# Performance work log

Measured on AMD Instinct MI355X. Metric: run time of the kernel, lower is better.

Reference implementation:

```python
import jax, jax.numpy as jnp
import numpy as np

MEL, EMB, PRE, RNN, ATT = 80, 256, 256, 1024, 128
LOC_FILTERS, LOC_KERNEL = 32, 31


def _dropout(x, p, key):
    keep = jax.random.bernoulli(key, 1.0 - p, x.shape)
    return jnp.where(keep, x / (1.0 - p), 0.0).astype(x.dtype)


def _lstm_cell(x, h, c, Wih, Whh, bih, bhh):
    # torch LSTMCell gate order: i, f, g, o
    gates = x @ Wih.T + h @ Whh.T + (bih + bhh)
    i, f, g, o = jnp.split(gates, 4, axis=-1)
    c_new = jax.nn.sigmoid(f) * c + jax.nn.sigmoid(i) * jnp.tanh(g)
    h_new = jax.nn.sigmoid(o) * jnp.tanh(c_new)
    return h_new, c_new


def setup_inputs() -> dict:
    key = jax.random.key(0)
    ks = jax.random.split(key, 24)
    r = lambda k, shape, fan: (jax.random.normal(k, shape, jnp.float32) / np.sqrt(fan))
    inp = {
        "embedding": jax.random.normal(ks[0], (32, 512, EMB), jnp.float32),
        "target_mels": jax.random.uniform(ks[1], (32, 400, MEL), jnp.float32),
        # PreNet
        "W1": r(ks[2], (PRE, MEL), MEL), "b1": jnp.zeros((PRE,), jnp.float32),
        "W2": r(ks[3], (PRE, PRE), PRE), "b2": jnp.zeros((PRE,), jnp.float32),
        # pre_rnn LSTMCell: input = pre_net_dim + embedding_dim = 512
        "Wih_pre": r(ks[4], (4 * RNN, PRE + EMB), PRE + EMB),
        "Whh_pre": r(ks[5], (4 * RNN, RNN), RNN),
        "bih_pre": jnp.zeros((4 * RNN,), jnp.float32),
        "bhh_pre": jnp.zeros((4 * RNN,), jnp.float32),
        # location-sensitive attention
        "Wq": r(ks[6], (ATT, RNN), RNN),
        "Wmem": r(ks[7], (ATT, EMB), EMB),
        "conv_w": r(ks[8], (LOC_FILTERS, 2, LOC_KERNEL), 2 * LOC_KERNEL),
        "Wloc": r(ks[9], (ATT, LOC_FILTERS), LOC_FILTERS),
        "v": r(ks[10], (ATT,), ATT),
        # post_rnn LSTMCell: input = rnn_dim + embedding_dim = 1280
        "Wih_post": r(ks[11], (4 * RNN, RNN + EMB), RNN + EMB),
        "Whh_post": r(ks[12], (4 * RNN, RNN), RNN),
        "bih_post": jnp.zeros((4 * RNN,), jnp.float32),
        "bhh_post": jnp.zeros((4 * RNN,), jnp.float32),
        # projections
        "Wmel": r(ks[13], (MEL, RNN + EMB), RNN + EMB), "bmel": jnp.zeros((MEL,), jnp.float32),
        "Wstop": r(ks[14], (1, RNN + EMB), RNN + EMB), "bstop": jnp.zeros((1,), jnp.float32),
    }
    return inp


def _decoder_forward(embedding, target_mels, W1, b1, W2, b2,
                     Wih_pre, Whh_pre, bih_pre, bhh_pre,
                     Wq, Wmem, conv_w, Wloc, v,
                     Wih_post, Whh_post, bih_post, bhh_post,
                     Wmel, bmel, Wstop, bstop):
    B, S, _ = embedding.shape
    T = target_mels.shape[1]
    # precompute processed memory [B, S, ATT]
    mem_proj = jnp.einsum("bse,ae->bsa", embedding, Wmem)
    # teacher-forced previous frames: zeros GO frame then target_mels[:, :-1]
    prev = jnp.concatenate([jnp.zeros((B, 1, MEL), target_mels.dtype), target_mels[:, :-1]], axis=1)
    prev = jnp.transpose(prev, (1, 0, 2))  # [T, B, MEL]
    base_key = jax.random.key(42)

    def step(carry, xs):
        c_pre, h_pre, c_post, h_post, context, a_w, a_sum = carry
        mel_prev, t = xs
        k1, k2, k3, k4 = jax.random.split(jax.random.fold_in(base_key, t), 4)
        # PreNet (dropout always on, p=0.5)
        p = _dropout(jax.nn.relu(mel_prev @ W1.T + b1), 0.5, k1)
        p = _dropout(jax.nn.relu(p @ W2.T + b2), 0.5, k2)
        # pre_rnn -- note original swaps (c, h) state names; replicated faithfully
        x = jnp.concatenate([p, context], axis=-1)
        c_pre, h_pre = _lstm_cell(x, c_pre, h_pre, Wih_pre, Whh_pre, bih_pre, bhh_pre)
        c_pre = _dropout(c_pre, 0.1, k3)
        # location-sensitive attention; query = h_pre (as in source)
        align_cat = jnp.stack([a_sum, a_w], axis=1)  # [B, 2, S]
        loc = jax.lax.conv_general_dilated(
            align_cat, conv_w, window_strides=(1,),
            padding=[(LOC_KERNEL // 2, LOC_KERNEL // 2)],
            dimension_numbers=("NCH", "OIH", "NCH"))  # [B, 32, S]
        q = h_pre @ Wq.T  # [B, ATT]
        loc_proj = jnp.einsum("bcs,ac->bsa", loc, Wloc)
        energies = jnp.einsum("bsa,a->bs", jnp.tanh(q[:, None, :] + mem_proj + loc_proj), v)
        a_w = jax.nn.softmax(energies, axis=-1)  # [B, S]
        context = jnp.einsum("bs,bse->be", a_w, embedding)
        a_sum = a_sum + a_w
        # post_rnn (same swapped-state convention)
        x2 = jnp.concatenate([h_pre, context], axis=-1)
        c_post, h_post = _lstm_cell(x2, c_post, h_post, Wih_post, Whh_post, bih_post, bhh_post)
        c_post = _dropout(c_post, 0.1, k4)
        out = jnp.concatenate([h_post, context], axis=-1)
        mel = jax.nn.sigmoid(out @ Wmel.T + bmel)
        stop = jax.nn.sigmoid(out @ Wstop.T + bstop)
        return (c_pre, h_pre, c_post, h_post, context, a_w, a_sum), (mel, stop)

    z = lambda d: jnp.zeros((B, d), embedding.dtype)
    carry0 = (z(RNN), z(RNN), z(RNN), z(RNN), z(EMB),
              jnp.zeros((B, S), embedding.dtype), jnp.zeros((B, S), embedding.dtype))
    _, (mels, stops) = jax.lax.scan(step, carry0, (prev, jnp.arange(T)))
    mel_frames = jnp.transpose(mels, (1, 0, 2))   # [B, T, MEL]
    stop_values = jnp.transpose(stops, (1, 0, 2))  # [B, T, 1]
    return mel_frames, stop_values


def reference(embedding, target_mels, W1, b1, W2, b2,
              Wih_pre, Whh_pre, bih_pre, bhh_pre,
              Wq, Wmem, conv_w, Wloc, v,
              Wih_post, Whh_post, bih_post, bhh_post,
              Wmel, bmel, Wstop, bstop):
    return _decoder_forward(embedding, target_mels, W1, b1, W2, b2,
                            Wih_pre, Whh_pre, bih_pre, bhh_pre,
                            Wq, Wmem, conv_w, Wloc, v,
                            Wih_post, Whh_post, bih_post, bhh_post,
                            Wmel, bmel, Wstop, bstop)
```

## Files before the change

### kernel.cpp

```cpp
#include <hip/hip_runtime.h>
#include <cstdint>
#include <cstddef>


#define JAX_THREEFRY_PARTITIONABLE 1

#define BB   32
#define SS   512
#define EMBD 256
#define MELD 80
#define PRED 256
#define RNND 1024
#define ATTD 128
#define TT   400

__device__ __forceinline__ void tf_block(uint32_t k0, uint32_t k1,
                                         uint32_t x0, uint32_t x1,
                                         uint32_t& o0, uint32_t& o1) {
  uint32_t ks2 = k0 ^ k1 ^ 0x1BD11BDAu;
  x0 += k0; x1 += k1;
#define TFR(r) { x0 += x1; x1 = (x1 << (r)) | (x1 >> (32 - (r))); x1 ^= x0; }
  TFR(13) TFR(15) TFR(26) TFR(6)
  x0 += k1;  x1 += ks2 + 1u;
  TFR(17) TFR(29) TFR(16) TFR(24)
  x0 += ks2; x1 += k0 + 2u;
  TFR(13) TFR(15) TFR(26) TFR(6)
  x0 += k0;  x1 += k1 + 3u;
  TFR(17) TFR(29) TFR(16) TFR(24)
  x0 += k1;  x1 += ks2 + 4u;
  TFR(13) TFR(15) TFR(26) TFR(6)
  x0 += ks2; x1 += k0 + 5u;
#undef TFR
  o0 = x0; o1 = x1;
}

__device__ __forceinline__ void subkey(int t, int j, uint32_t& k0, uint32_t& k1) {
  uint32_t a, b;
  tf_block(0u, 42u, 0u, (uint32_t)t, a, b);
#if JAX_THREEFRY_PARTITIONABLE
  tf_block(a, b, 0u, (uint32_t)j, k0, k1);
#else
  uint32_t base = (uint32_t)((j & 1) * 2);
  uint32_t w = (uint32_t)(j >> 1);
  uint32_t p0, p1, q0, q1;
  tf_block(a, b, base,     base + 4u, p0, p1);
  tf_block(a, b, base + 1u, base + 5u, q0, q1);
  k0 = w ? p1 : p0;
  k1 = w ? q1 : q0;
#endif
}

__device__ __forceinline__ bool keep_draw(uint32_t k0, uint32_t k1,
                                          uint32_t idx, uint32_t n, float pkeep) {
  uint32_t bits;
#if JAX_THREEFRY_PARTITIONABLE
  uint32_t o0, o1;
  tf_block(k0, k1, 0u, idx, o0, o1);
  bits = o0 ^ o1;
#else
  uint32_t half = n >> 1;
  uint32_t o0, o1;
  if (idx < half) { tf_block(k0, k1, idx, idx + half, o0, o1); bits = o0; }
  else            { tf_block(k0, k1, idx - half, idx, o0, o1); bits = o1; }
#endif
  float u = __uint_as_float((bits >> 9) | 0x3f800000u) - 1.0f;
  return u < pkeep;
}

__device__ __forceinline__ float sigm(float x) { return 1.0f / (1.0f + expf(-x)); }

__global__ void zero_kernel(float* p, int n) {
  int i = blockIdx.x * blockDim.x + threadIdx.x;
  if (i < n) p[i] = 0.0f;
}

__global__ __launch_bounds__(256) void prenet_kernel(
    const float* __restrict__ tmels, const float* __restrict__ W1,
    const float* __restrict__ b1, const float* __restrict__ W2,
    const float* __restrict__ b2, float* __restrict__ P_all) {
  __shared__ float melsh[MELD];
  __shared__ float h1sh[PRED];
  int blk = blockIdx.x, tid = threadIdx.x;
  int t = blk >> 5, b = blk & 31;
  if (tid < MELD)
    melsh[tid] = (t == 0) ? 0.0f : tmels[((size_t)b * TT + (t - 1)) * MELD + tid];
  __syncthreads();
  uint32_t k10, k11, k20, k21;
  subkey(t, 0, k10, k11);
  subkey(t, 1, k20, k21);
  {
    const float* wr = W1 + (size_t)tid * MELD;
    float acc = b1[tid];
    for (int m = 0; m < MELD; ++m) acc += melsh[m] * wr[m];
    acc = fmaxf(acc, 0.0f);
    bool kp = keep_draw(k10, k11, (uint32_t)(b * PRED + tid), BB * PRED, 0.5f);
    h1sh[tid] = kp ? (acc / 0.5f) : 0.0f;
  }
  __syncthreads();
  {
    const float* wr = W2 + (size_t)tid * PRED;
    float acc = b2[tid];
    for (int k = 0; k < PRED; ++k) acc += h1sh[k] * wr[k];
    acc = fmaxf(acc, 0.0f);
    bool kp = keep_draw(k20, k21, (uint32_t)(b * PRED + tid), BB * PRED, 0.5f);
    P_all[((size_t)t * BB + b) * PRED + tid] = kp ? (acc / 0.5f) : 0.0f;
  }
}

__global__ __launch_bounds__(128) void memproj_kernel(
    const float* __restrict__ emb, const float* __restrict__ Wmem,
    float* __restrict__ mp) {
  __shared__ float esh[EMBD];
  int blk = blockIdx.x, tid = threadIdx.x;
  const float* er = emb + (size_t)blk * EMBD;
  esh[tid] = er[tid];
  esh[tid + 128] = er[tid + 128];
  __syncthreads();
  const float4* wr = (const float4*)(Wmem + (size_t)tid * EMBD);
  const float4* xr = (const float4*)esh;
  float acc = 0.0f;
  for (int k4 = 0; k4 < EMBD / 4; ++k4) {
    float4 w = wr[k4], x = xr[k4];
    acc += w.x * x.x + w.y * x.y + w.z * x.z + w.w * x.w;
  }
  mp[(size_t)blk * ATTD + tid] = acc;
}

__global__ __launch_bounds__(256) void combo_kernel(
    int t, int do1, int do2,
    const float* __restrict__ P_all,
    const float* __restrict__ ctx_r,
    const float* __restrict__ Apre_r, const float* __restrict__ Bpre_r,
    float* __restrict__ Apre_w, float* __restrict__ Bpre_w,
    const float* __restrict__ Wih_pre, const float* __restrict__ Whh_pre,
    const float* __restrict__ bih_pre, const float* __restrict__ bhh_pre,
    const float* __restrict__ Apost_r, const float* __restrict__ Bpost_r,
    float* __restrict__ Apost_w, float* __restrict__ Bpost_w,
    const float* __restrict__ Wih_post, const float* __restrict__ Whh_post,
    const float* __restrict__ bih_post, const float* __restrict__ bhh_post) {
  __shared__ float xs[BB][256];
  const int blk = blockIdx.x;
  const int tid = threadIdx.x;
  const bool is1 = (blk < 128);
  if (is1 ? !do1 : !do2) return;
  const int tstep = is1 ? t : (t - 1);
  const int hb = (is1 ? blk : blk - 128) * 8;
  const int col = tid & 31;
  const int lq  = tid >> 5;
  const int b0  = lq * 4;
  const int gate = col >> 3;
  const int hl   = col & 7;
  const int gcol = gate * RNND + hb + hl;
  const int nchunks = is1 ? 6 : 9;

  float acc0 = 0.f, acc1 = 0.f, acc2 = 0.f, acc3 = 0.f;

  for (int ch = 0; ch < nchunks; ++ch) {
    __syncthreads();
#pragma unroll
    for (int it = 0; it < 8; ++it) {
      int flat = tid + it * 256;
      int bb = flat >> 6;
      int k4 = flat & 63;
      const float* src;
      if (is1) {
        if (ch == 0)      src = P_all + ((size_t)t * BB + bb) * PRED;
        else if (ch == 1) src = ctx_r + (size_t)bb * EMBD;
        else              src = Apre_r + (size_t)bb * RNND + (ch - 2) * 256;
      } else {
        if (ch < 4)       src = Bpre_r + (size_t)bb * RNND + ch * 256;
        else if (ch == 4) src = ctx_r + (size_t)bb * EMBD;
        else              src = Apost_r + (size_t)bb * RNND + (ch - 5) * 256;
      }
      float4 v4 = *(((const float4*)src) + k4);
      *(((float4*)&xs[bb][0]) + k4) = v4;
    }
    __syncthreads();

    const float* wrow;
    if (is1) wrow = (ch < 2) ? (Wih_pre + (size_t)gcol * 512 + ch * 256)
                             : (Whh_pre + (size_t)gcol * 1024 + (ch - 2) * 256);
    else     wrow = (ch < 5) ? (Wih_post + (size_t)gcol * 1280 + ch * 256)
                             : (Whh_post + (size_t)gcol * 1024 + (ch - 5) * 256);
    const float4* w4p = (const float4*)wrow;
#pragma unroll 8
    for (int k4 = 0; k4 < 64; ++k4) {
      float4 w = w4p[k4];
      float4 xa = *(((const float4*)&xs[b0 + 0][0]) + k4);
      float4 xb = *(((const float4*)&xs[b0 + 1][0]) + k4);
      float4 xc = *(((const float4*)&xs[b0 + 2][0]) + k4);
      float4 xd = *(((const float4*)&xs[b0 + 3][0]) + k4);
      acc0 += w.x * xa.x + w.y * xa.y + w.z * xa.z + w.w * xa.w;
      acc1 += w.x * xb.x + w.y * xb.y + w.z * xb.z + w.w * xb.w;
      acc2 += w.x * xc.x + w.y * xc.y + w.z * xc.z + w.w * xc.w;
      acc3 += w.x * xd.x + w.y * xd.y + w.z * xd.z + w.w * xd.w;
    }
  }

  float bsum = is1 ? (bih_pre[gcol] + bhh_pre[gcol])
                   : (bih_post[gcol] + bhh_post[gcol]);
  acc0 += bsum; acc1 += bsum; acc2 += bsum; acc3 += bsum;

  int lane = tid & 63;
  float f0 = __shfl(acc0, lane + 8),  f1 = __shfl(acc1, lane + 8);
  float f2 = __shfl(acc2, lane + 8),  f3 = __shfl(acc3, lane + 8);
  float g0 = __shfl(acc0, lane + 16), g1 = __shfl(acc1, lane + 16);
  float g2 = __shfl(acc2, lane + 16), g3 = __shfl(acc3, lane + 16);
  float q0 = __shfl(acc0, lane + 24), q1 = __shfl(acc1, lane + 24);
  float q2 = __shfl(acc2, lane + 24), q3 = __shfl(acc3, lane + 24);

  if (gate == 0) {
    uint32_t kk0, kk1;
    subkey(tstep, is1 ? 2 : 3, kk0, kk1);
    const int h = hb + hl;
    const float* Bold = is1 ? Bpre_r : Bpost_r;
    float* Aw = is1 ? Apre_w : Apost_w;
    float* Bw = is1 ? Bpre_w : Bpost_w;
    float ia[4] = {acc0, acc1, acc2, acc3};
    float fa[4] = {f0, f1, f2, f3};
    float ga[4] = {g0, g1, g2, g3};
    float oa[4] = {q0, q1, q2, q3};
#pragma unroll
    for (int i2 = 0; i2 < 4; ++i2) {
      int bb = b0 + i2;
      float iv = sigm(ia[i2]);
      float fv = sigm(fa[i2]);
      float gv = tanhf(ga[i2]);
      float ov = sigm(oa[i2]);
      float c_new = fv * Bold[(size_t)bb * RNND + h] + iv * gv;
      float h_new = ov * tanhf(c_new);
      bool kp = keep_draw(kk0, kk1, (uint32_t)(bb * RNND + h), BB * RNND, 0.9f);
      Aw[(size_t)bb * RNND + h] = kp ? (h_new / 0.9f) : 0.0f;
      Bw[(size_t)bb * RNND + h] = c_new;
    }
  }
}

__global__ __launch_bounds__(256) void q_kernel(
    const float* __restrict__ Bpre_new, const float* __restrict__ Wq,
    float* __restrict__ qout) {
  __shared__ float xsh[2][RNND];
  int blk = blockIdx.x, tid = threadIdx.x;
  int b2 = blk * 2;
  for (int flat = tid; flat < 2 * RNND; flat += 256)
    xsh[flat >> 10][flat & 1023] =
        Bpre_new[(size_t)(b2 + (flat >> 10)) * RNND + (flat & 1023)];
  __syncthreads();
  int a = tid & 127, bh = tid >> 7;
  const float4* wr = (const float4*)(Wq + (size_t)a * RNND);
  const float4* xr = (const float4*)&xsh[bh][0];
  float acc = 0.0f;
  for (int k4 = 0; k4 < RNND / 4; ++k4) {
    float4 w = wr[k4], x = xr[k4];
    acc += w.x * x.x + w.y * x.y + w.z * x.z + w.w * x.w;
  }
  qout[(size_t)(b2 + bh) * ATTD + a] = acc;
}

__global__ __launch_bounds__(256) void att_kernel(
    int do_att, int do_out, int t_prev,
    const float* __restrict__ qin, const float* __restrict__ memproj,
    const float* __restrict__ aw_r, const float* __restrict__ asum_r,
    const float* __restrict__ conv_w, const float* __restrict__ Wloc,
    const float* __restrict__ vvec, float* __restrict__ energ,
    const float* __restrict__ Bpost_o, const float* __restrict__ ctx_o,
    const float* __restrict__ Wmel, const float* __restrict__ bmel,
    const float* __restrict__ Wstop, const float* __restrict__ bstop,
    float* __restrict__ dout) {
  int blk = blockIdx.x, tid = threadIdx.x;
  if (blk >= 256) {
    if (!do_out) return;
    int b = blk - 256;
    int o = tid;
    if (o > 80) return;
    const float* wrow = (o < 80) ? (Wmel + (size_t)o * 1280) : Wstop;
    const float4* w4 = (const float4*)wrow;
    const float4* x4 = (const float4*)(Bpost_o + (size_t)b * RNND);
    float acc = 0.0f;
    for (int k4 = 0; k4 < RNND / 4; ++k4) {
      float4 w = w4[k4], x = x4[k4];
      acc += w.x * x.x + w.y * x.y + w.z * x.z + w.w * x.w;
    }
    const float4* w4b = (const float4*)(wrow + RNND);
    const float4* c4 = (const float4*)(ctx_o + (size_t)b * EMBD);
    for (int k4 = 0; k4 < EMBD / 4; ++k4) {
      float4 w = w4b[k4], x = c4[k4];
      acc += w.x * x.x + w.y * x.y + w.z * x.z + w.w * x.w;
    }
    acc += (o < 80) ? bmel[o] : bstop[0];
    float val = sigm(acc);
    if (o < 80) dout[(size_t)b * (TT * MELD) + (size_t)t_prev * MELD + o] = val;
    else        dout[(size_t)BB * TT * MELD + (size_t)b * TT + t_prev] = val;
    return;
  }
  if (!do_att) return;
  __shared__ float qsh[ATTD];
  __shared__ float vsh[ATTD];
  __shared__ float awin[94], aswin[94];
  __shared__ float wlocs[ATTD * 33];
  __shared__ float convs[32 * 62];
  __shared__ float locs[64 * 33];
  int b = blk >> 3, st = blk & 7, s0 = st * 64;
  if (tid < ATTD) { qsh[tid] = qin[b * ATTD + tid]; vsh[tid] = vvec[tid]; }
  if (tid < 94) {
    int sg = s0 - 15 + tid;
    bool ok = (sg >= 0) && (sg < SS);
    awin[tid]  = ok ? aw_r[b * SS + sg]   : 0.0f;
    aswin[tid] = ok ? asum_r[b * SS + sg] : 0.0f;
  }
  for (int idx = tid; idx < ATTD * 32; idx += 256) {
    int a = idx >> 5, c = idx & 31;
    wlocs[a * 33 + c] = Wloc[a * 32 + c];
  }
  for (int idx = tid; idx < 32 * 62; idx += 256) convs[idx] = conv_w[idx];
  __syncthreads();
  for (int idx = tid; idx < 64 * 32; idx += 256) {
    int sl = idx & 63, c = idx >> 6;
    const float* cw0 = &convs[c * 62];
    const float* cw1 = &convs[c * 62 + 31];
    float acc = 0.0f;
    for (int k = 0; k < 31; ++k)
      acc += cw0[k] * aswin[sl + k] + cw1[k] * awin[sl + k];
    locs[sl * 33 + c] = acc;
  }
  __syncthreads();
  int sl = tid >> 2, aq = tid & 3, sg = s0 + sl;
  const float* mp = memproj + ((size_t)b * SS + sg) * ATTD;
  float acc = 0.0f;
  const float* ls = &locs[sl * 33];
  for (int j = 0; j < 32; ++j) {
    int a = j * 4 + aq;
    const float* wl = &wlocs[a * 33];
    float lp = 0.0f;
#pragma unroll 8
    for (int c = 0; c < 32; ++c) lp += ls[c] * wl[c];
    acc += vsh[a] * tanhf(qsh[a] + mp[a] + lp);
  }
  acc += __shfl_down(acc, 2);
  acc += __shfl_down(acc, 1);
  if (aq == 0) energ[b * SS + sg] = acc;
}

__global__ __launch_bounds__(256) void sm_ctx_kernel(
    const float* __restrict__ energ, const float* __restrict__ emb,
    const float* __restrict__ asum_r, float* __restrict__ aw_w,
    float* __restrict__ asum_w, float* __restrict__ ctx_w) {
  __shared__ float psh[SS];
  __shared__ float red[256];
  __shared__ float cpart[4][64];
  int blk = blockIdx.x, tid = threadIdx.x;
  int b = blk >> 2, ec = blk & 3;
  float e1 = energ[b * SS + tid], e2 = energ[b * SS + 256 + tid];
  red[tid] = fmaxf(e1, e2);
  __syncthreads();
  for (int s = 128; s > 0; s >>= 1) {
    if (tid < s) red[tid] = fmaxf(red[tid], red[tid + s]);
    __syncthreads();
  }
  float mx = red[0];
  __syncthreads();
  float p1 = expf(e1 - mx), p2 = expf(e2 - mx);
  psh[tid] = p1; psh[tid + 256] = p2;
  red[tid] = p1 + p2;
  __syncthreads();
  for (int s = 128; s > 0; s >>= 1) {
    if (tid < s) red[tid] += red[tid + s];
    __syncthreads();
  }
  float inv = 1.0f / red[0];
  int el = tid & 63, sq = tid >> 6;
  int e = ec * 64 + el;
  float acc = 0.0f;
  const float* ebase = emb + ((size_t)b * SS) * EMBD + e;
  for (int s = sq * 128; s < sq * 128 + 128; ++s)
    acc += psh[s] * ebase[(size_t)s * EMBD];
  cpart[sq][el] = acc;
  __syncthreads();
  if (tid < 64)
    ctx_w[b * EMBD + ec * 64 + tid] =
        (cpart[0][tid] + cpart[1][tid] + cpart[2][tid] + cpart[3][tid]) * inv;
  if (ec == 0) {
    float a1 = p1 * inv, a2 = p2 * inv;
    aw_w[b * SS + tid] = a1;
    aw_w[b * SS + 256 + tid] = a2;
    asum_w[b * SS + tid] = asum_r[b * SS + tid] + a1;
    asum_w[b * SS + 256 + tid] = asum_r[b * SS + 256 + tid] + a2;
  }
}

extern "C" void kernel_launch(void* const* d_in, const int* in_sizes, int n_in,
                              void* d_out, int out_size, void* d_ws, size_t ws_size,
                              hipStream_t stream) {
  const float* emb      = (const float*)d_in[0];
  const float* tmels    = (const float*)d_in[1];
  const float* W1       = (const float*)d_in[2];
  const float* b1       = (const float*)d_in[3];
  const float* W2       = (const float*)d_in[4];
  const float* b2       = (const float*)d_in[5];
  const float* Wih_pre  = (const float*)d_in[6];
  const float* Whh_pre  = (const float*)d_in[7];
  const float* bih_pre  = (const float*)d_in[8];
  const float* bhh_pre  = (const float*)d_in[9];
  const float* Wq       = (const float*)d_in[10];
  const float* Wmem     = (const float*)d_in[11];
  const float* conv_w   = (const float*)d_in[12];
  const float* Wloc     = (const float*)d_in[13];
  const float* vvec     = (const float*)d_in[14];
  const float* Wih_post = (const float*)d_in[15];
  const float* Whh_post = (const float*)d_in[16];
  const float* bih_post = (const float*)d_in[17];
  const float* bhh_post = (const float*)d_in[18];
  const float* Wmel     = (const float*)d_in[19];
  const float* bmel     = (const float*)d_in[20];
  const float* Wstop    = (const float*)d_in[21];
  const float* bstop    = (const float*)d_in[22];
  float* out = (float*)d_out;

  float* w = (float*)d_ws;
  size_t off = 0;
  auto carve = [&](size_t n) {
    float* p = w + off;
    off += (n + 63) & ~((size_t)63);
    return p;
  };
  float* memproj = carve((size_t)BB * SS * ATTD);
  float* P_all   = carve((size_t)TT * BB * PRED);
  size_t state_begin = off;
  float* Apre[2]  = {carve(BB * RNND), carve(BB * RNND)};
  float* Bpre[2]  = {carve(BB * RNND), carve(BB * RNND)};
  float* Apost[2] = {carve(BB * RNND), carve(BB * RNND)};
  float* Bpost[2] = {carve(BB * RNND), carve(BB * RNND)};
  float* ctx[2]   = {carve(BB * EMBD), carve(BB * EMBD)};
  float* aw[2]    = {carve(BB * SS), carve(BB * SS)};
  float* asum[2]  = {carve(BB * SS), carve(BB * SS)};
  size_t state_end = off;
  float* q     = carve(BB * ATTD);
  float* energ = carve(BB * SS);

  int nz = (int)(state_end - state_begin);
  zero_kernel<<<(nz + 255) / 256, 256, 0, stream>>>(w + state_begin, nz);

  prenet_kernel<<<TT * BB, 256, 0, stream>>>(tmels, W1, b1, W2, b2, P_all);
  memproj_kernel<<<BB * SS, 128, 0, stream>>>(emb, Wmem, memproj);

  for (int t = 0; t <= TT; ++t) {
    int r = t & 1, wr2 = 1 - r;
    combo_kernel<<<256, 256, 0, stream>>>(
        t, (int)(t < TT), (int)(t > 0),
        P_all, ctx[r], Apre[r], Bpre[r], Apre[wr2], Bpre[wr2],
        Wih_pre, Whh_pre, bih_pre, bhh_pre,
        Apost[wr2], Bpost[wr2], Apost[r], Bpost[r],
        Wih_post, Whh_post, bih_post, bhh_post);
    if (t < TT) {
      q_kernel<<<16, 256, 0, stream>>>(Bpre[wr2], Wq, q);
      att_kernel<<<288, 256, 0, stream>>>(
          1, (int)(t > 0), t - 1,
          q, memproj, aw[r], asum[r], conv_w, Wloc, vvec, energ,
          Bpost[r], ctx[r], Wmel, bmel, Wstop, bstop, out);
      sm_ctx_kernel<<<128, 256, 0, stream>>>(
          energ, emb, asum[r], aw[wr2], asum[wr2], ctx[wr2]);
    } else {
      att_kernel<<<288, 256, 0, stream>>>(
          0, 1, t - 1,
          q, memproj, aw[r], asum[r], conv_w, Wloc, vvec, energ,
          Bpost[r], ctx[r], Wmel, bmel, Wstop, bstop, out);
    }
  }
  (void)in_sizes; (void)n_in; (void)out_size; (void)ws_size;
}
```

Before: 79.72 ms.

## Fuse per-step decoder kernels into one persistent kernel with grid barriers

Replaces the roughly 1600 per-timestep kernel launches (combo, q, attention, softmax/context) with a single persistent 256-block kernel. It loops over timesteps internally and separates phases with an atomic-counter grid barrier. The goal is to remove per-launch overhead and inter-kernel gaps on this latency-bound recurrent loop. It relies on all 256 blocks being co-resident, and the spin barriers add their own synchronisation cost. The non-partitionable threefry path is also removed.

```diff
diff --git a/kernel.cpp b/kernel.cpp
--- a/kernel.cpp
+++ b/kernel.cpp
@@ -2,8 +2,6 @@
 #include <cstdint>
 #include <cstddef>
 
-
-#define JAX_THREEFRY_PARTITIONABLE 1
 
 #define BB   32
 #define SS   512
@@ -13,6 +11,7 @@
 #define RNND 1024
 #define ATTD 128
 #define TT   400
+#define NBLK 256
 
 __device__ __forceinline__ void tf_block(uint32_t k0, uint32_t k1,
                                          uint32_t x0, uint32_t x1,
@@ -37,41 +36,44 @@
 __device__ __forceinline__ void subkey(int t, int j, uint32_t& k0, uint32_t& k1) {
   uint32_t a, b;
   tf_block(0u, 42u, 0u, (uint32_t)t, a, b);
-#if JAX_THREEFRY_PARTITIONABLE
   tf_block(a, b, 0u, (uint32_t)j, k0, k1);
-#else
-  uint32_t base = (uint32_t)((j & 1) * 2);
-  uint32_t w = (uint32_t)(j >> 1);
-  uint32_t p0, p1, q0, q1;
-  tf_block(a, b, base,     base + 4u, p0, p1);
-  tf_block(a, b, base + 1u, base + 5u, q0, q1);
-  k0 = w ? p1 : p0;
-  k1 = w ? q1 : q0;
-#endif
 }
 
 __device__ __forceinline__ bool keep_draw(uint32_t k0, uint32_t k1,
-                                          uint32_t idx, uint32_t n, float pkeep) {
-  uint32_t bits;
-#if JAX_THREEFRY_PARTITIONABLE
+                                          uint32_t idx, float pkeep) {
   uint32_t o0, o1;
   tf_block(k0, k1, 0u, idx, o0, o1);
-  bits = o0 ^ o1;
-#else
-  uint32_t half = n >> 1;
-  uint32_t o0, o1;
-  if (idx < half) { tf_block(k0, k1, idx, idx + half, o0, o1); bits = o0; }
-  else            { tf_block(k0, k1, idx - half, idx, o0, o1); bits = o1; }
-#endif
+  uint32_t bits = o0 ^ o1;
   float u = __uint_as_float((bits >> 9) | 0x3f800000u) - 1.0f;
   return u < pkeep;
 }
 
 __device__ __forceinline__ float sigm(float x) { return 1.0f / (1.0f + expf(-x)); }
 
-__global__ void zero_kernel(float* p, int n) {
+__device__ __forceinline__ void gsync(uint32_t* cnt, uint32_t* gen, uint32_t& lgen) {
+  __threadfence();
+  __syncthreads();
+  lgen += 1u;
+  if (threadIdx.x == 0) {
+    uint32_t a = __hip_atomic_fetch_add(cnt, 1u, __ATOMIC_ACQ_REL,
+                                        __HIP_MEMORY_SCOPE_AGENT);
+    if (a == (uint32_t)(NBLK - 1)) {
+      __hip_atomic_store(cnt, 0u, __ATOMIC_RELAXED, __HIP_MEMORY_SCOPE_AGENT);
+      __hip_atomic_store(gen, lgen, __ATOMIC_RELEASE, __HIP_MEMORY_SCOPE_AGENT);
+    } else {
+      while (__hip_atomic_load(gen, __ATOMIC_ACQUIRE,
+                               __HIP_MEMORY_SCOPE_AGENT) < lgen) {
+        __builtin_amdgcn_s_sleep(2);
+      }
+    }
+  }
+  __syncthreads();
+}
+
+__global__ void init_kernel(float* statebase, int nstate, uint32_t* barrier2) {
   int i = blockIdx.x * blockDim.x + threadIdx.x;
-  if (i < n) p[i] = 0.0f;
+  if (i < nstate) statebase[i] = 0.0f;
+  if (i == 0) { barrier2[0] = 0u; barrier2[1] = 0u; }
 }
 
 __global__ __launch_bounds__(256) void prenet_kernel(
@@ -93,7 +95,7 @@
     float acc = b1[tid];
     for (int m = 0; m < MELD; ++m) acc += melsh[m] * wr[m];
     acc = fmaxf(acc, 0.0f);
-    bool kp = keep_draw(k10, k11, (uint32_t)(b * PRED + tid), BB * PRED, 0.5f);
+    bool kp = keep_draw(k10, k11, (uint32_t)(b * PRED + tid), 0.5f);
     h1sh[tid] = kp ? (acc / 0.5f) : 0.0f;
   }
   __syncthreads();
@@ -102,7 +104,7 @@
     float acc = b2[tid];
     for (int k = 0; k < PRED; ++k) acc += h1sh[k] * wr[k];
     acc = fmaxf(acc, 0.0f);
-    bool kp = keep_draw(k20, k21, (uint32_t)(b * PRED + tid), BB * PRED, 0.5f);
+    bool kp = keep_draw(k20, k21, (uint32_t)(b * PRED + tid), 0.5f);
     P_all[((size_t)t * BB + b) * PRED + tid] = kp ? (acc / 0.5f) : 0.0f;
   }
 }
@@ -126,345 +128,348 @@
   mp[(size_t)blk * ATTD + tid] = acc;
 }
 
-__global__ __launch_bounds__(256) void combo_kernel(
-    int t, int do1, int do2,
-    const float* __restrict__ P_all,
-    const float* __restrict__ ctx_r,
-    const float* __restrict__ Apre_r, const float* __restrict__ Bpre_r,
-    float* __restrict__ Apre_w, float* __restrict__ Bpre_w,
-    const float* __restrict__ Wih_pre, const float* __restrict__ Whh_pre,
-    const float* __restrict__ bih_pre, const float* __restrict__ bhh_pre,
-    const float* __restrict__ Apost_r, const float* __restrict__ Bpost_r,
-    float* __restrict__ Apost_w, float* __restrict__ Bpost_w,
-    const float* __restrict__ Wih_post, const float* __restrict__ Whh_post,
-    const float* __restrict__ bih_post, const float* __restrict__ bhh_post) {
-  __shared__ float xs[BB][256];
+struct DecParams {
+  const float *emb, *tmels;
+  const float *Wih_pre, *Whh_pre, *bih_pre, *bhh_pre;
+  const float *Wq, *conv_w, *Wloc, *vvec;
+  const float *Wih_post, *Whh_post, *bih_post, *bhh_post;
+  const float *Wmel, *bmel, *Wstop, *bstop;
+  float *out;
+  float *memproj, *P_all;
+  float *Apre0, *Apre1, *Bpre0, *Bpre1;
+  float *Apost0, *Apost1, *Bpost0, *Bpost1;
+  float *ctx0, *ctx1, *aw0, *aw1, *asum0, *asum1;
+  float *qbuf, *energ;
+  uint32_t *barrier2;
+};
+
+__global__ __launch_bounds__(256) void decoder_persistent(DecParams p) {
+  __shared__ __align__(16) float smem[8768];
   const int blk = blockIdx.x;
   const int tid = threadIdx.x;
-  const bool is1 = (blk < 128);
-  if (is1 ? !do1 : !do2) return;
-  const int tstep = is1 ? t : (t - 1);
-  const int hb = (is1 ? blk : blk - 128) * 8;
-  const int col = tid & 31;
-  const int lq  = tid >> 5;
-  const int b0  = lq * 4;
-  const int gate = col >> 3;
-  const int hl   = col & 7;
-  const int gcol = gate * RNND + hb + hl;
-  const int nchunks = is1 ? 6 : 9;
-
-  float acc0 = 0.f, acc1 = 0.f, acc2 = 0.f, acc3 = 0.f;
-
-  for (int ch = 0; ch < nchunks; ++ch) {
-    __syncthreads();
+  uint32_t* bcnt = p.barrier2;
+  uint32_t* bgen = p.barrier2 + 1;
+  uint32_t lgen = 0u;
+
+  for (int t = 0; t <= TT; ++t) {
+    const int rr = t & 1;
+    const float* Apre_r  = rr ? p.Apre1  : p.Apre0;
+    const float* Bpre_r  = rr ? p.Bpre1  : p.Bpre0;
+    float*       Apre_w  = rr ? p.Apre0  : p.Apre1;
+    float*       Bpre_w  = rr ? p.Bpre0  : p.Bpre1;
+    const float* Apost_r = rr ? p.Apost0 : p.Apost1;
+    const float* Bpost_r = rr ? p.Bpost0 : p.Bpost1;
+    float*       Apost_w = rr ? p.Apost1 : p.Apost0;
+    float*       Bpost_w = rr ? p.Bpost1 : p.Bpost0;
+    const float* ctx_r   = rr ? p.ctx1   : p.ctx0;
+    float*       ctx_w   = rr ? p.ctx0   : p.ctx1;
+    const float* aw_r    = rr ? p.aw1    : p.aw0;
+    float*       aw_w    = rr ? p.aw0    : p.aw1;
+    const float* asum_r  = rr ? p.asum1  : p.asum0;
+    float*       asum_w  = rr ? p.asum0  : p.asum1;
+
+    {
+      const bool is1 = (blk < 128);
+      const bool active = is1 ? (t < TT) : (t > 0);
+      if (active) {
+        float (*xs)[256] = (float (*)[256])smem;
+        const int tstep = is1 ? t : (t - 1);
+        const int hb = (is1 ? blk : blk - 128) * 8;
+        const int col = tid & 31;
+        const int lq  = tid >> 5;
+        const int b0  = lq * 4;
+        const int gate = col >> 3;
+        const int hl   = col & 7;
+        const int gcol = gate * RNND + hb + hl;
+        const int nchunks = is1 ? 6 : 9;
+
+        float acc0 = 0.f, acc1 = 0.f, acc2 = 0.f, acc3 = 0.f;
+
+        for (int ch = 0; ch < nchunks; ++ch) {
+          __syncthreads();
 #pragma unroll
-    for (int it = 0; it < 8; ++it) {
-      int flat = tid + it * 256;
-      int bb = flat >> 6;
-      int k4 = flat & 63;
-      const float* src;
-      if (is1) {
-        if (ch == 0)      src = P_all + ((size_t)t * BB + bb) * PRED;
-        else if (ch == 1) src = ctx_r + (size_t)bb * EMBD;
-        else              src = Apre_r + (size_t)bb * RNND + (ch - 2) * 256;
-      } else {
-        if (ch < 4)       src = Bpre_r + (size_t)bb * RNND + ch * 256;
-        else if (ch == 4) src = ctx_r + (size_t)bb * EMBD;
-        else              src = Apost_r + (size_t)bb * RNND + (ch - 5) * 256;
-      }
-      float4 v4 = *(((const float4*)src) + k4);
-      *(((float4*)&xs[bb][0]) + k4) = v4;
+          for (int it = 0; it < 8; ++it) {
+            int flat = tid + it * 256;
+            int bb = flat >> 6;
+            int k4 = flat & 63;
+            const float* src;
+            if (is1) {
+              if (ch == 0)      src = p.P_all + ((size_t)t * BB + bb) * PRED;
+              else if (ch == 1) src = ctx_r + (size_t)bb * EMBD;
+              else              src = Apre_r + (size_t)bb * RNND + (ch - 2) * 256;
+            } else {
+              if (ch < 4)       src = Bpre_r + (size_t)bb * RNND + ch * 256;
+              else if (ch == 4) src = ctx_r + (size_t)bb * EMBD;
+              else              src = Apost_r + (size_t)bb * RNND + (ch - 5) * 256;
+            }
+            float4 v4 = *(((const float4*)src) + k4);
+            *(((float4*)&xs[bb][0]) + k4) = v4;
+          }
+          __syncthreads();
+
+          const float* wrow;
+          if (is1) wrow = (ch < 2) ? (p.Wih_pre + (size_t)gcol * 512 + ch * 256)
+                                   : (p.Whh_pre + (size_t)gcol * 1024 + (ch - 2) * 256);
+          else     wrow = (ch < 5) ? (p.Wih_post + (size_t)gcol * 1280 + ch * 256)
+                                   : (p.Whh_post + (size_t)gcol * 1024 + (ch - 5) * 256);
+          const float4* w4p = (const float4*)wrow;
+#pragma unroll 8
+          for (int k4 = 0; k4 < 64; ++k4) {
+            float4 w = w4p[k4];
+            float4 xa = *(((const float4*)&xs[b0 + 0][0]) + k4);
+            float4 xb = *(((const float4*)&xs[b0 + 1][0]) + k4);
+            float4 xc = *(((const float4*)&xs[b0 + 2][0]) + k4);
+            float4 xd = *(((const float4*)&xs[b0 + 3][0]) + k4);
+            acc0 += w.x * xa.x + w.y * xa.y + w.z * xa.z + w.w * xa.w;
+            acc1 += w.x * xb.x + w.y * xb.y + w.z * xb.z + w.w * xb.w;
+            acc2 += w.x * xc.x + w.y * xc.y + w.z * xc.z + w.w * xc.w;
+            acc3 += w.x * xd.x + w.y * xd.y + w.z * xd.z + w.w * xd.w;
+          }
+        }
+
+        float bsum = is1 ? (p.bih_pre[gcol] + p.bhh_pre[gcol])
+                         : (p.bih_post[gcol] + p.bhh_post[gcol]);
+        acc0 += bsum; acc1 += bsum; acc2 += bsum; acc3 += bsum;
+
+        int lane = tid & 63;
+        float f0 = __shfl(acc0, lane + 8),  f1 = __shfl(acc1, lane + 8);
+        float f2 = __shfl(acc2, lane + 8),  f3 = __shfl(acc3, lane + 8);
+        float g0 = __shfl(acc0, lane + 16), g1 = __shfl(acc1, lane + 16);
+        float g2 = __shfl(acc2, lane + 16), g3 = __shfl(acc3, lane + 16);
+        float q0 = __shfl(acc0, lane + 24), q1 = __shfl(acc1, lane + 24);
+        float q2 = __shfl(acc2, lane + 24), q3 = __shfl(acc3, lane + 24);
+
+        if (gate == 0) {
+          uint32_t kk0, kk1;
+          subkey(tstep, is1 ? 2 : 3, kk0, kk1);
+          const int h = hb + hl;
+          const float* Bold = is1 ? Bpre_r : Bpost_r;
+          float* Aw = is1 ? Apre_w : Apost_w;
+          float* Bw = is1 ? Bpre_w : Bpost_w;
+          float ia[4] = {acc0, acc1, acc2, acc3};
+          float fa[4] = {f0, f1, f2, f3};
+          float ga[4] = {g0, g1, g2, g3};
+          float oa[4] = {q0, q1, q2, q3};
+#pragma unroll
+          for (int i2 = 0; i2 < 4; ++i2) {
+            int bb = b0 + i2;
+            float iv = sigm(ia[i2]);
+            float fv = sigm(fa[i2]);
+            float gv = tanhf(ga[i2]);
+            float ov = sigm(oa[i2]);
+            float c_new = fv * Bold[(size_t)bb * RNND + h] + iv * gv;
+            float h_new = ov * tanhf(c_new);
+            bool kp = keep_draw(kk0, kk1, (uint32_t)(bb * RNND + h), 0.9f);
+            Aw[(size_t)bb * RNND + h] = kp ? (h_new / 0.9f) : 0.0f;
+            Bw[(size_t)bb * RNND + h] = c_new;
+          }
+        }
+      }
     }
-    __syncthreads();
-
-    const float* wrow;
-    if (is1) wrow = (ch < 2) ? (Wih_pre + (size_t)gcol * 512 + ch * 256)
-                             : (Whh_pre + (size_t)gcol * 1024 + (ch - 2) * 256);
-    else     wrow = (ch < 5) ? (Wih_post + (size_t)gcol * 1280 + ch * 256)
-                             : (Whh_post + (size_t)gcol * 1024 + (ch - 5) * 256);
-    const float4* w4p = (const float4*)wrow;
+    gsync(bcnt, bgen, lgen);
+
+    if (blk < 16) {
+      if (t < TT) {
+        float* xsh = smem;
+        int b2 = blk * 2;
+        for (int flat = tid; flat < 2 * RNND; flat += 256)
+          xsh[flat] = Bpre_w[(size_t)(b2 + (flat >> 10)) * RNND + (flat & 1023)];
+        __syncthreads();
+        int a = tid & 127, bh = tid >> 7;
+        const float4* wr = (const float4*)(p.Wq + (size_t)a * RNND);
+        const float4* xr = ((const float4*)xsh) + bh * (RNND / 4);
+        float acc = 0.0f;
+        for (int k4 = 0; k4 < RNND / 4; ++k4) {
+          float4 w = wr[k4], x = xr[k4];
+          acc += w.x * x.x + w.y * x.y + w.z * x.z + w.w * x.w;
+        }
+        p.qbuf[(size_t)(b2 + bh) * ATTD + a] = acc;
+      }
+    } else if (blk < 48) {
+      if (t > 0) {
+        int b = blk - 16;
+        int o = tid;
+        int t_prev = t - 1;
+        if (o <= 80) {
+          const float* wrow = (o < 80) ? (p.Wmel + (size_t)o * 1280) : p.Wstop;
+          const float4* w4 = (const float4*)wrow;
+          const float4* x4 = (const float4*)(Bpost_w + (size_t)b * RNND);
+          float acc = 0.0f;
+          for (int k4 = 0; k4 < RNND / 4; ++k4) {
+            float4 w = w4[k4], x = x4[k4];
+            acc += w.x * x.x + w.y * x.y + w.z * x.z + w.w * x.w;
+          }
+          const float4* w4b = (const float4*)(wrow + RNND);
+          const float4* c4 = (const float4*)(ctx_r + (size_t)b * EMBD);
+          for (int k4 = 0; k4 < EMBD / 4; ++k4) {
+            float4 w = w4b[k4], x = c4[k4];
+            acc += w.x * x.x + w.y * x.y + w.z * x.z + w.w * x.w;
+          }
+          acc += (o < 80) ? p.bmel[o] : p.bstop[0];
+          float val = sigm(acc);
+          if (o < 80)
+            p.out[(size_t)b * (TT * MELD) + (size_t)t_prev * MELD + o] = val;
+          else
+            p.out[(size_t)BB * TT * MELD + (size_t)b * TT + t_prev] = val;
+        }
+      }
+    }
+    gsync(bcnt, bgen, lgen);
+
+    if (t < TT) {
+      float* qsh   = smem;
+      float* vsh   = smem + 128;
+      float* awin  = smem + 256;
+      float* aswin = smem + 352;
+      float* wlocs = smem + 448;
+      float* convs = smem + 4672;
+      float* locs  = smem + 6656;
+      int b = blk >> 3, st = blk & 7, s0 = st * 64;
+      __syncthreads();
+      if (tid < ATTD) { qsh[tid] = p.qbuf[b * ATTD + tid]; vsh[tid] = p.vvec[tid]; }
+      if (tid < 94) {
+        int sg = s0 - 15 + tid;
+        bool ok = (sg >= 0) && (sg < SS);
+        awin[tid]  = ok ? aw_r[b * SS + sg]   : 0.0f;
+        aswin[tid] = ok ? asum_r[b * SS + sg] : 0.0f;
+      }
+      for (int idx = tid; idx < ATTD * 32; idx += 256) {
+        int a = idx >> 5, c = idx & 31;
+        wlocs[a * 33 + c] = p.Wloc[a * 32 + c];
+      }
+      for (int idx = tid; idx < 32 * 62; idx += 256) convs[idx] = p.conv_w[idx];
+      __syncthreads();
+      for (int idx = tid; idx < 64 * 32; idx += 256) {
+        int sl = idx & 63, c = idx >> 6;
+        const float* cw0 = &convs[c * 62];
+        const float* cw1 = &convs[c * 62 + 31];
+        float acc = 0.0f;
+        for (int k = 0; k < 31; ++k)
+          acc += cw0[k] * aswin[sl + k] + cw1[k] * awin[sl + k];
+        locs[sl * 33 + c] = acc;
+      }
+      __syncthreads();
+      int sl = tid >> 2, aq = tid & 3, sg = s0 + sl;
+      const float* mp = p.memproj + ((size_t)b * SS + sg) * ATTD;
+      float acc = 0.0f;
+      const float* ls = &locs[sl * 33];
+      for (int j = 0; j < 32; ++j) {
+        int a = j * 4 + aq;
+        const float* wl = &wlocs[a * 33];
+        float lp = 0.0f;
 #pragma unroll 8
-    for (int k4 = 0; k4 < 64; ++k4) {
-      float4 w = w4p[k4];
-      float4 xa = *(((const float4*)&xs[b0 + 0][0]) + k4);
-      float4 xb = *(((const float4*)&xs[b0 + 1][0]) + k4);
-      float4 xc = *(((const float4*)&xs[b0 + 2][0]) + k4);
-      float4 xd = *(((const float4*)&xs[b0 + 3][0]) + k4);
-      acc0 += w.x * xa.x + w.y * xa.y + w.z * xa.z + w.w * xa.w;
-      acc1 += w.x * xb.x + w.y * xb.y + w.z * xb.z + w.w * xb.w;
-      acc2 += w.x * xc.x + w.y * xc.y + w.z * xc.z + w.w * xc.w;
-      acc3 += w.x * xd.x + w.y * xd.y + w.z * xd.z + w.w * xd.w;
+        for (int c = 0; c < 32; ++c) lp += ls[c] * wl[c];
+        acc += vsh[a] * tanhf(qsh[a] + mp[a] + lp);
+      }
+      acc += __shfl_down(acc, 2);
+      acc += __shfl_down(acc, 1);
+      if (aq == 0) p.energ[b * SS + sg] = acc;
     }
-  }
-
-  float bsum = is1 ? (bih_pre[gcol] + bhh_pre[gcol])
-                   : (bih_post[gcol] + bhh_post[gcol]);
-  acc0 += bsum; acc1 += bsum; acc2 += bsum; acc3 += bsum;
-
-  int lane = tid & 63;
-  float f0 = __shfl(acc0, lane + 8),  f1 = __shfl(acc1, lane + 8);
-  float f2 = __shfl(acc2, lane + 8),  f3 = __shfl(acc3, lane + 8);
-  float g0 = __shfl(acc0, lane + 16), g1 = __shfl(acc1, lane + 16);
-  float g2 = __shfl(acc2, lane + 16), g3 = __shfl(acc3, lane + 16);
-  float q0 = __shfl(acc0, lane + 24), q1 = __shfl(acc1, lane + 24);
-  float q2 = __shfl(acc2, lane + 24), q3 = __shfl(acc3, lane + 24);
-
-  if (gate == 0) {
-    uint32_t kk0, kk1;
-    subkey(tstep, is1 ? 2 : 3, kk0, kk1);
-    const int h = hb + hl;
-    const float* Bold = is1 ? Bpre_r : Bpost_r;
-    float* Aw = is1 ? Apre_w : Apost_w;
-    float* Bw = is1 ? Bpre_w : Bpost_w;
-    float ia[4] = {acc0, acc1, acc2, acc3};
-    float fa[4] = {f0, f1, f2, f3};
-    float ga[4] = {g0, g1, g2, g3};
-    float oa[4] = {q0, q1, q2, q3};
-#pragma unroll
-    for (int i2 = 0; i2 < 4; ++i2) {
-      int bb = b0 + i2;
-      float iv = sigm(ia[i2]);
-      float fv = sigm(fa[i2]);
-      float gv = tanhf(ga[i2]);
-      float ov = sigm(oa[i2]);
-      float c_new = fv * Bold[(size_t)bb * RNND + h] + iv * gv;
-      float h_new = ov * tanhf(c_new);
-      bool kp = keep_draw(kk0, kk1, (uint32_t)(bb * RNND + h), BB * RNND, 0.9f);
-      Aw[(size_t)bb * RNND + h] = kp ? (h_new / 0.9f) : 0.0f;
-      Bw[(size_t)bb * RNND + h] = c_new;
+    gsync(bcnt, bgen, lgen);
+
+    if (t < TT && blk < 128) {
+      float* psh   = smem;
+      float* red   = smem + 512;
+      float (*cpart)[64] = (float (*)[64])(smem + 768);
+      int b = blk >> 2, ec = blk & 3;
+      float e1 = p.energ[b * SS + tid], e2 = p.energ[b * SS + 256 + tid];
+      red[tid] = fmaxf(e1, e2);
+      __syncthreads();
+      for (int s = 128; s > 0; s >>= 1) {
+        if (tid < s) red[tid] = fmaxf(red[tid], red[tid + s]);
+        __syncthreads();
+      }
+      float mx = red[0];
+      __syncthreads();
+      float p1 = expf(e1 - mx), p2 = expf(e2 - mx);
+      psh[tid] = p1; psh[tid + 256] = p2;
+      red[tid] = p1 + p2;
+      __syncthreads();
+      for (int s = 128; s > 0; s >>= 1) {
+        if (tid < s) red[tid] += red[tid + s];
+        __syncthreads();
+      }
+      float inv = 1.0f / red[0];
+      int el = tid & 63, sq = tid >> 6;
+      int e = ec * 64 + el;
+      float acc = 0.0f;
+      const float* ebase = p.emb + ((size_t)b * SS) * EMBD + e;
+      for (int s = sq * 128; s < sq * 128 + 128; ++s)
+        acc += psh[s] * ebase[(size_t)s * EMBD];
+      cpart[sq][el] = acc;
+      __syncthreads();
+      if (tid < 64)
+        ctx_w[b * EMBD + ec * 64 + tid] =
+            (cpart[0][tid] + cpart[1][tid] + cpart[2][tid] + cpart[3][tid]) * inv;
+      if (ec == 0) {
+        float a1 = p1 * inv, a2 = p2 * inv;
+        aw_w[b * SS + tid] = a1;
+        aw_w[b * SS + 256 + tid] = a2;
+        asum_w[b * SS + tid] = asum_r[b * SS + tid] + a1;
+        asum_w[b * SS + 256 + tid] = asum_r[b * SS + 256 + tid] + a2;
+      }
     }
-  }
-}
-
-__global__ __launch_bounds__(256) void q_kernel(
-    const float* __restrict__ Bpre_new, const float* __restrict__ Wq,
-    float* __restrict__ qout) {
-  __shared__ float xsh[2][RNND];
-  int blk = blockIdx.x, tid = threadIdx.x;
-  int b2 = blk * 2;
-  for (int flat = tid; flat < 2 * RNND; flat += 256)
-    xsh[flat >> 10][flat & 1023] =
-        Bpre_new[(size_t)(b2 + (flat >> 10)) * RNND + (flat & 1023)];
-  __syncthreads();
-  int a = tid & 127, bh = tid >> 7;
-  const float4* wr = (const float4*)(Wq + (size_t)a * RNND);
-  const float4* xr = (const float4*)&xsh[bh][0];
-  float acc = 0.0f;
-  for (int k4 = 0; k4 < RNND / 4; ++k4) {
-    float4 w = wr[k4], x = xr[k4];
-    acc += w.x * x.x + w.y * x.y + w.z * x.z + w.w * x.w;
-  }
-  qout[(size_t)(b2 + bh) * ATTD + a] = acc;
-}
-
-__global__ __launch_bounds__(256) void att_kernel(
-    int do_att, int do_out, int t_prev,
-    const float* __restrict__ qin, const float* __restrict__ memproj,
-    const float* __restrict__ aw_r, const float* __restrict__ asum_r,
-    const float* __restrict__ conv_w, const float* __restrict__ Wloc,
-    const float* __restrict__ vvec, float* __restrict__ energ,
-    const float* __restrict__ Bpost_o, const float* __restrict__ ctx_o,
-    const float* __restrict__ Wmel, const float* __restrict__ bmel,
-    const float* __restrict__ Wstop, const float* __restrict__ bstop,
-    float* __restrict__ dout) {
-  int blk = blockIdx.x, tid = threadIdx.x;
-  if (blk >= 256) {
-    if (!do_out) return;
-    int b = blk - 256;
-    int o = tid;
-    if (o > 80) return;
-    const float* wrow = (o < 80) ? (Wmel + (size_t)o * 1280) : Wstop;
-    const float4* w4 = (const float4*)wrow;
-    const float4* x4 = (const float4*)(Bpost_o + (size_t)b * RNND);
-    float acc = 0.0f;
-    for (int k4 = 0; k4 < RNND / 4; ++k4) {
-      float4 w = w4[k4], x = x4[k4];
-      acc += w.x * x.x + w.y * x.y + w.z * x.z + w.w * x.w;
-    }
-    const float4* w4b = (const float4*)(wrow + RNND);
-    const float4* c4 = (const float4*)(ctx_o + (size_t)b * EMBD);
-    for (int k4 = 0; k4 < EMBD / 4; ++k4) {
-      float4 w = w4b[k4], x = c4[k4];
-      acc += w.x * x.x + w.y * x.y + w.z * x.z + w.w * x.w;
-    }
-    acc += (o < 80) ? bmel[o] : bstop[0];
-    float val = sigm(acc);
-    if (o < 80) dout[(size_t)b * (TT * MELD) + (size_t)t_prev * MELD + o] = val;
-    else        dout[(size_t)BB * TT * MELD + (size_t)b * TT + t_prev] = val;
-    return;
-  }
-  if (!do_att) return;
-  __shared__ float qsh[ATTD];
-  __shared__ float vsh[ATTD];
-  __shared__ float awin[94], aswin[94];
-  __shared__ float wlocs[ATTD * 33];
-  __shared__ float convs[32 * 62];
-  __shared__ float locs[64 * 33];
-  int b = blk >> 3, st = blk & 7, s0 = st * 64;
-  if (tid < ATTD) { qsh[tid] = qin[b * ATTD + tid]; vsh[tid] = vvec[tid]; }
-  if (tid < 94) {
-    int sg = s0 - 15 + tid;
-    bool ok = (sg >= 0) && (sg < SS);
-    awin[tid]  = ok ? aw_r[b * SS + sg]   : 0.0f;
-    aswin[tid] = ok ? asum_r[b * SS + sg] : 0.0f;
-  }
-  for (int idx = tid; idx < ATTD * 32; idx += 256) {
-    int a = idx >> 5, c = idx & 31;
-    wlocs[a * 33 + c] = Wloc[a * 32 + c];
-  }
-  for (int idx = tid; idx < 32 * 62; idx += 256) convs[idx] = conv_w[idx];
-  __syncthreads();
-  for (int idx = tid; idx < 64 * 32; idx += 256) {
-    int sl = idx & 63, c = idx >> 6;
-    const float* cw0 = &convs[c * 62];
-    const float* cw1 = &convs[c * 62 + 31];
-    float acc = 0.0f;
-    for (int k = 0; k < 31; ++k)
-      acc += cw0[k] * aswin[sl + k] + cw1[k] * awin[sl + k];
-    locs[sl * 33 + c] = acc;
-  }
-  __syncthreads();
-  int sl = tid >> 2, aq = tid & 3, sg = s0 + sl;
-  const float* mp = memproj + ((size_t)b * SS + sg) * ATTD;
-  float acc = 0.0f;
-  const float* ls = &locs[sl * 33];
-  for (int j = 0; j < 32; ++j) {
-    int a = j * 4 + aq;
-    const float* wl = &wlocs[a * 33];
-    float lp = 0.0f;
-#pragma unroll 8
-    for (int c = 0; c < 32; ++c) lp += ls[c] * wl[c];
-    acc += vsh[a] * tanhf(qsh[a] + mp[a] + lp);
-  }
-  acc += __shfl_down(acc, 2);
-  acc += __shfl_down(acc, 1);
-  if (aq == 0) energ[b * SS + sg] = acc;
-}
-
-__global__ __launch_bounds__(256) void sm_ctx_kernel(
-    const float* __restrict__ energ, const float* __restrict__ emb,
-    const float* __restrict__ asum_r, float* __restrict__ aw_w,
-    float* __restrict__ asum_w, float* __restrict__ ctx_w) {
-  __shared__ float psh[SS];
-  __shared__ float red[256];
-  __shared__ float cpart[4][64];
-  int blk = blockIdx.x, tid = threadIdx.x;
-  int b = blk >> 2, ec = blk & 3;
-  float e1 = energ[b * SS + tid], e2 = energ[b * SS + 256 + tid];
-  red[tid] = fmaxf(e1, e2);
-  __syncthreads();
-  for (int s = 128; s > 0; s >>= 1) {
-    if (tid < s) red[tid] = fmaxf(red[tid], red[tid + s]);
-    __syncthreads();
-  }
-  float mx = red[0];
-  __syncthreads();
-  float p1 = expf(e1 - mx), p2 = expf(e2 - mx);
-  psh[tid] = p1; psh[tid + 256] = p2;
-  red[tid] = p1 + p2;
-  __syncthreads();
-  for (int s = 128; s > 0; s >>= 1) {
-    if (tid < s) red[tid] += red[tid + s];
-    __syncthreads();
-  }
-  float inv = 1.0f / red[0];
-  int el = tid & 63, sq = tid >> 6;
-  int e = ec * 64 + el;
-  float acc = 0.0f;
-  const float* ebase = emb + ((size_t)b * SS) * EMBD + e;
-  for (int s = sq * 128; s < sq * 128 + 128; ++s)
-    acc += psh[s] * ebase[(size_t)s * EMBD];
-  cpart[sq][el] = acc;
-  __syncthreads();
-  if (tid < 64)
-    ctx_w[b * EMBD + ec * 64 + tid] =
-        (cpart[0][tid] + cpart[1][tid] + cpart[2][tid] + cpart[3][tid]) * inv;
-  if (ec == 0) {
-    float a1 = p1 * inv, a2 = p2 * inv;
-    aw_w[b * SS + tid] = a1;
-    aw_w[b * SS + 256 + tid] = a2;
-    asum_w[b * SS + tid] = asum_r[b * SS + tid] + a1;
-    asum_w[b * SS + 256 + tid] = asum_r[b * SS + 256 + tid] + a2;
+    gsync(bcnt, bgen, lgen);
   }
 }
 
 extern "C" void kernel_launch(void* const* d_in, const int* in_sizes, int n_in,
                               void* d_out, int out_size, void* d_ws, size_t ws_size,
                               hipStream_t stream) {
-  const float* emb      = (const float*)d_in[0];
-  const float* tmels    = (const float*)d_in[1];
-  const float* W1       = (const float*)d_in[2];
-  const float* b1       = (const float*)d_in[3];
-  const float* W2       = (const float*)d_in[4];
-  const float* b2       = (const float*)d_in[5];
-  const float* Wih_pre  = (const float*)d_in[6];
-  const float* Whh_pre  = (const float*)d_in[7];
-  const float* bih_pre  = (const float*)d_in[8];
-  const float* bhh_pre  = (const float*)d_in[9];
-  const float* Wq       = (const float*)d_in[10];
-  const float* Wmem     = (const float*)d_in[11];
-  const float* conv_w   = (const float*)d_in[12];
-  const float* Wloc     = (const float*)d_in[13];
-  const float* vvec     = (const float*)d_in[14];
-  const float* Wih_post = (const float*)d_in[15];
-  const float* Whh_post = (const float*)d_in[16];
-  const float* bih_post = (const float*)d_in[17];
-  const float* bhh_post = (const float*)d_in[18];
-  const float* Wmel     = (const float*)d_in[19];
-  const float* bmel     = (const float*)d_in[20];
-  const float* Wstop    = (const float*)d_in[21];
-  const float* bstop    = (const float*)d_in[22];
-  float* out = (float*)d_out;
+  DecParams hp;
+  hp.emb      = (const float*)d_in[0];
+  hp.tmels    = (const float*)d_in[1];
+  const float* W1 = (const float*)d_in[2];
+  const float* b1 = (const float*)d_in[3];
+  const float* W2 = (const float*)d_in[4];
+  const float* b2 = (const float*)d_in[5];
+  hp.Wih_pre  = (const float*)d_in[6];
+  hp.Whh_pre  = (const float*)d_in[7];
+  hp.bih_pre  = (const float*)d_in[8];
+  hp.bhh_pre  = (const float*)d_in[9];
+  hp.Wq       = (const float*)d_in[10];
+  const float* Wmem = (const float*)d_in[11];
+  hp.conv_w   = (const float*)d_in[12];
+  hp.Wloc     = (const float*)d_in[13];
+  hp.vvec     = (const float*)d_in[14];
+  hp.Wih_post = (const float*)d_in[15];
+  hp.Whh_post = (const float*)d_in[16];
+  hp.bih_post = (const float*)d_in[17];
+  hp.bhh_post = (const float*)d_in[18];
+  hp.Wmel     = (const float*)d_in[19];
+  hp.bmel     = (const float*)d_in[20];
+  hp.Wstop    = (const float*)d_in[21];
+  hp.bstop    = (const float*)d_in[22];
+  hp.out = (float*)d_out;
 
   float* w = (float*)d_ws;
   size_t off = 0;
   auto carve = [&](size_t n) {
-    float* p = w + off;
+    float* ptr = w + off;
     off += (n + 63) & ~((size_t)63);
-    return p;
+    return ptr;
   };
-  float* memproj = carve((size_t)BB * SS * ATTD);
-  float* P_all   = carve((size_t)TT * BB * PRED);
+  hp.memproj = carve((size_t)BB * SS * ATTD);
+  hp.P_all   = carve((size_t)TT * BB * PRED);
   size_t state_begin = off;
-  float* Apre[2]  = {carve(BB * RNND), carve(BB * RNND)};
-  float* Bpre[2]  = {carve(BB * RNND), carve(BB * RNND)};
-  float* Apost[2] = {carve(BB * RNND), carve(BB * RNND)};
-  float* Bpost[2] = {carve(BB * RNND), carve(BB * RNND)};
-  float* ctx[2]   = {carve(BB * EMBD), carve(BB * EMBD)};
-  float* aw[2]    = {carve(BB * SS), carve(BB * SS)};
-  float* asum[2]  = {carve(BB * SS), carve(BB * SS)};
+  hp.Apre0  = carve(BB * RNND); hp.Apre1  = carve(BB * RNND);
+  hp.Bpre0  = carve(BB * RNND); hp.Bpre1  = carve(BB * RNND);
+  hp.Apost0 = carve(BB * RNND); hp.Apost1 = carve(BB * RNND);
+  hp.Bpost0 = carve(BB * RNND); hp.Bpost1 = carve(BB * RNND);
+  hp.ctx0   = carve(BB * EMBD); hp.ctx1   = carve(BB * EMBD);
+  hp.aw0    = carve(BB * SS);   hp.aw1    = carve(BB * SS);
+  hp.asum0  = carve(BB * SS);   hp.asum1  = carve(BB * SS);
   size_t state_end = off;
-  float* q     = carve(BB * ATTD);
-  float* energ = carve(BB * SS);
-
-  int nz = (int)(state_end - state_begin);
-  zero_kernel<<<(nz + 255) / 256, 256, 0, stream>>>(w + state_begin, nz);
-
-  prenet_kernel<<<TT * BB, 256, 0, stream>>>(tmels, W1, b1, W2, b2, P_all);
-  memproj_kernel<<<BB * SS, 128, 0, stream>>>(emb, Wmem, memproj);
-
-  for (int t = 0; t <= TT; ++t) {
-    int r = t & 1, wr2 = 1 - r;
-    combo_kernel<<<256, 256, 0, stream>>>(
-        t, (int)(t < TT), (int)(t > 0),
-        P_all, ctx[r], Apre[r], Bpre[r], Apre[wr2], Bpre[wr2],
-        Wih_pre, Whh_pre, bih_pre, bhh_pre,
-        Apost[wr2], Bpost[wr2], Apost[r], Bpost[r],
-        Wih_post, Whh_post, bih_post, bhh_post);
-    if (t < TT) {
-      q_kernel<<<16, 256, 0, stream>>>(Bpre[wr2], Wq, q);
-      att_kernel<<<288, 256, 0, stream>>>(
-          1, (int)(t > 0), t - 1,
-          q, memproj, aw[r], asum[r], conv_w, Wloc, vvec, energ,
-          Bpost[r], ctx[r], Wmel, bmel, Wstop, bstop, out);
-      sm_ctx_kernel<<<128, 256, 0, stream>>>(
-          energ, emb, asum[r], aw[wr2], asum[wr2], ctx[wr2]);
-    } else {
-      att_kernel<<<288, 256, 0, stream>>>(
-          0, 1, t - 1,
-          q, memproj, aw[r], asum[r], conv_w, Wloc, vvec, energ,
-          Bpost[r], ctx[r], Wmel, bmel, Wstop, bstop, out);
-    }
-  }
+  hp.qbuf  = carve(BB * ATTD);
+  hp.energ = carve(BB * SS);
+  hp.barrier2 = (uint32_t*)carve(64);
+  int nstate = (int)(state_end - state_begin);
+
+  init_kernel<<<(nstate + 255) / 256, 256, 0, stream>>>(
+      w + state_begin, nstate, hp.barrier2);
+  prenet_kernel<<<TT * BB, 256, 0, stream>>>(hp.tmels, W1, b1, W2, b2, hp.P_all);
+  memproj_kernel<<<BB * SS, 128, 0, stream>>>(hp.emb, Wmem, hp.memproj);
+  decoder_persistent<<<NBLK, 256, 0, stream>>>(hp);
+
   (void)in_sizes; (void)n_in; (void)out_size; (void)ws_size;
 }
```

Result: slower. 172.2 ms (+116.1%).
